# Optimization experiments

Measured on AMD Instinct MI355X. Metric: run time of the kernel, lower is better.

The kernel has to match this reference:

```python
import jax, jax.numpy as jnp
import numpy as np

N_NODES = 40000


def _sage_conv(x, edge_index, W_l, W_r, b, num_nodes):
    # PyG SAGEConv (mean aggr): out = lin_l(mean_{j in N(i)} x_j) + lin_r(x_i)
    src, dst = edge_index[0], edge_index[1]
    msgs = x[src]                                            # [E, F] gather
    sums = jax.ops.segment_sum(msgs, dst, num_segments=num_nodes)
    counts = jax.ops.segment_sum(jnp.ones((src.shape[0],), x.dtype), dst,
                                 num_segments=num_nodes)
    mean = sums / jnp.maximum(counts, 1.0)[:, None]          # [N, F]
    return mean @ W_l + b + x @ W_r


def setup_inputs() -> dict:
    key = jax.random.key(0)
    ks = jax.random.split(key, 8)
    in_c, hid_c, out_c = 128, 256, 128
    x = jax.random.normal(ks[0], (N_NODES, in_c), dtype=jnp.float32)
    edge_index = jax.random.randint(ks[1], (2, 640000), 0, N_NODES, dtype=jnp.int64)
    s1 = 1.0 / np.sqrt(in_c)
    s2 = 1.0 / np.sqrt(hid_c)
    return {
        "x": x,
        "edge_index": edge_index,
        "W1_l": jax.random.uniform(ks[2], (in_c, hid_c), jnp.float32, -s1, s1),
        "W1_r": jax.random.uniform(ks[3], (in_c, hid_c), jnp.float32, -s1, s1),
        "b1": jnp.zeros((hid_c,), jnp.float32),
        "W2_l": jax.random.uniform(ks[4], (hid_c, out_c), jnp.float32, -s2, s2),
        "W2_r": jax.random.uniform(ks[5], (hid_c, out_c), jnp.float32, -s2, s2),
        "b2": jnp.zeros((out_c,), jnp.float32),
    }


def reference(x, edge_index, W1_l, W1_r, b1, W2_l, W2_r, b2):
    h = _sage_conv(x, edge_index, W1_l, W1_r, b1, N_NODES)
    h = jax.nn.relu(h)
    out = _sage_conv(h, edge_index, W2_l, W2_r, b2, N_NODES)
    return out
```

## Files before the change

### kernel.cpp

```cpp
#include <hip/hip_runtime.h>


constexpr int F1  = 128;
constexpr int HID = 256;

typedef __attribute__((ext_vector_type(8))) short   short8;
typedef __attribute__((ext_vector_type(8))) ushort  us8;
typedef __attribute__((ext_vector_type(4))) ushort  us4;
typedef __attribute__((ext_vector_type(4))) float   f32x4;

__device__ __forceinline__ ushort f2bf(float f) {
  unsigned u = __float_as_uint(f);
  return (ushort)((u + 0x7fffu + ((u >> 16) & 1u)) >> 16);
}
__device__ __forceinline__ float bf2f_lo(unsigned v) { return __uint_as_float(v << 16); }
__device__ __forceinline__ float bf2f_hi(unsigned v) { return __uint_as_float(v & 0xffff0000u); }

__global__ void prep_kernel(const float* __restrict__ x, ushort* __restrict__ Ab,
                            int* __restrict__ deg,
                            const float* __restrict__ W1l, const float* __restrict__ W1r,
                            const float* __restrict__ W2l, const float* __restrict__ W2r,
                            ushort* __restrict__ B1t, ushort* __restrict__ B2t, int N) {
  int i = blockIdx.x * blockDim.x + threadIdx.x;
  if (i < N) deg[i] = 0;
  if (i < N * 16) {
    int row = i >> 4, c = (i & 15) * 8;
    const float* p = x + (size_t)row * F1 + c;
    us8 o;
#pragma unroll
    for (int j = 0; j < 8; ++j) o[j] = f2bf(p[j]);
    *(us8*)(Ab + (size_t)row * HID + 128 + c) = o;
    return;
  }
  int j = i - N * 16;
  if (j >= 16384) return;
  int which = j >> 13;
  int jj = j & 8191;
  int n = jj >> 5;
  int kb = (jj & 31) * 8;
  us8 o;
  if (which == 0) {
#pragma unroll
    for (int q = 0; q < 8; ++q) {
      int k = kb + q;
      float v = (k < 128) ? W1l[k * HID + n] : W1r[(k - 128) * HID + n];
      o[q] = f2bf(v);
    }
    *(us8*)(B1t + n * HID + kb) = o;
  } else {
#pragma unroll
    for (int q = 0; q < 8; ++q) {
      int k = kb + q;
      float v = (n < 128) ? W2l[k * F1 + n] : W2r[k * F1 + (n - 128)];
      o[q] = f2bf(v);
    }
    *(us8*)(B2t + n * HID + kb) = o;
  }
}

__global__ void deg_kernel(const int* __restrict__ dst, int* __restrict__ deg, int E) {
  int i = (blockIdx.x * blockDim.x + threadIdx.x) * 4;
  if (i + 3 < E) {
    int4 d = *(const int4*)(dst + i);
    atomicAdd(deg + d.x, 1);
    atomicAdd(deg + d.y, 1);
    atomicAdd(deg + d.z, 1);
    atomicAdd(deg + d.w, 1);
  } else {
    for (int q = i; q < E && q < i + 4; ++q) atomicAdd(deg + dst[q], 1);
  }
}

__global__ __launch_bounds__(256) void scan_part(const int* __restrict__ deg,
                                                 int* __restrict__ bsum, int N) {
  __shared__ int sm[256];
  int t = threadIdx.x;
  int base = blockIdx.x * 1024 + t * 4;
  int s = 0;
  if (base + 3 < N) {
    int4 v = *(const int4*)(deg + base);
    s = v.x + v.y + v.z + v.w;
  } else {
    for (int q = 0; q < 4; ++q) if (base + q < N) s += deg[base + q];
  }
  sm[t] = s;
  __syncthreads();
  for (int d = 128; d; d >>= 1) {
    if (t < d) sm[t] += sm[t + d];
    __syncthreads();
  }
  if (t == 0) bsum[blockIdx.x] = sm[0];
}

__global__ __launch_bounds__(256) void scan_emit(const int* __restrict__ deg,
                                                 const int* __restrict__ bsum,
                                                 int* __restrict__ off,
                                                 int* __restrict__ cursor, int N, int nb) {
  __shared__ int sm[256];
  __shared__ int sboff;
  int t = threadIdx.x;
  if (t < 64) {
    int v = (t < nb) ? bsum[t] : 0;
    int inc = v;
    for (int d = 1; d < 64; d <<= 1) {
      int u = __shfl_up(inc, d);
      if (t >= d) inc += u;
    }
    if (t == (int)blockIdx.x) sboff = inc - v;
    if ((int)blockIdx.x == (int)gridDim.x - 1 && t == 63) off[N] = inc;
  }
  int base = blockIdx.x * 1024 + t * 4;
  int d0 = 0, d1 = 0, d2 = 0, d3 = 0;
  if (base + 3 < N) {
    int4 v = *(const int4*)(deg + base);
    d0 = v.x; d1 = v.y; d2 = v.z; d3 = v.w;
  } else {
    if (base + 0 < N) d0 = deg[base + 0];
    if (base + 1 < N) d1 = deg[base + 1];
    if (base + 2 < N) d2 = deg[base + 2];
    if (base + 3 < N) d3 = deg[base + 3];
  }
  int s = d0 + d1 + d2 + d3;
  sm[t] = s;
  __syncthreads();
  for (int d = 1; d < 256; d <<= 1) {
    int u = (t >= d) ? sm[t - d] : 0;
    __syncthreads();
    sm[t] += u;
    __syncthreads();
  }
  int o0 = (t ? sm[t - 1] : 0) + sboff;
  int o1 = o0 + d0, o2 = o1 + d1, o3 = o2 + d2;
  if (base + 3 < N) {
    int4 o = make_int4(o0, o1, o2, o3);
    *(int4*)(off + base) = o;
    *(int4*)(cursor + base) = o;
  } else {
    if (base + 0 < N) { off[base + 0] = o0; cursor[base + 0] = o0; }
    if (base + 1 < N) { off[base + 1] = o1; cursor[base + 1] = o1; }
    if (base + 2 < N) { off[base + 2] = o2; cursor[base + 2] = o2; }
    if (base + 3 < N) { off[base + 3] = o3; cursor[base + 3] = o3; }
  }
}

__global__ void fill_kernel(const int* __restrict__ src, const int* __restrict__ dst,
                            int* __restrict__ cursor, int* __restrict__ csr, int E) {
  int i = (blockIdx.x * blockDim.x + threadIdx.x) * 2;
  if (i + 1 < E) {
    int2 d = *(const int2*)(dst + i);
    int2 s = *(const int2*)(src + i);
    int p0 = atomicAdd(cursor + d.x, 1);
    csr[p0] = s.x;
    int p1 = atomicAdd(cursor + d.y, 1);
    csr[p1] = s.y;
  } else if (i < E) {
    int p = atomicAdd(cursor + dst[i], 1);
    csr[p] = src[i];
  }
}

__device__ __forceinline__ void acc8(float* acc, const uint4 v) {
  acc[0] += bf2f_lo(v.x); acc[1] += bf2f_hi(v.x);
  acc[2] += bf2f_lo(v.y); acc[3] += bf2f_hi(v.y);
  acc[4] += bf2f_lo(v.z); acc[5] += bf2f_hi(v.z);
  acc[6] += bf2f_lo(v.w); acc[7] += bf2f_hi(v.w);
}

__global__ __launch_bounds__(256) void agg1_kernel(const int* __restrict__ off,
                                                   const int* __restrict__ csr,
                                                   ushort* __restrict__ Ab, int N) {
  const int t = threadIdx.x;
  const int w = t >> 6, l = t & 63;
  const int g = l >> 4, sub = l & 15;
  const int node = blockIdx.x * 16 + w * 4 + g;
  if (node >= N) return;
  const int s = off[node], e = off[node + 1];
  float acc[8] = {0.f, 0.f, 0.f, 0.f, 0.f, 0.f, 0.f, 0.f};
  const int cb = sub * 8;
  const int4* csr4 = (const int4*)csr;
  int k0 = s & ~7;
  int4 c0 = csr4[(k0 >> 2) + 0];
  int4 c1 = csr4[(k0 >> 2) + 1];
#define ROW1(j) (*(const uint4*)(Ab + (size_t)(j) * HID + 128 + cb))
  for (int k = k0; k < e; k += 8) {
    int4 n0 = csr4[(k >> 2) + 2];
    int4 n1 = csr4[(k >> 2) + 3];
    if (k + 0 >= s && k + 0 < e) acc8(acc, ROW1(c0.x));
    if (k + 1 >= s && k + 1 < e) acc8(acc, ROW1(c0.y));
    if (k + 2 >= s && k + 2 < e) acc8(acc, ROW1(c0.z));
    if (k + 3 >= s && k + 3 < e) acc8(acc, ROW1(c0.w));
    if (k + 4 >= s && k + 4 < e) acc8(acc, ROW1(c1.x));
    if (k + 5 >= s && k + 5 < e) acc8(acc, ROW1(c1.y));
    if (k + 6 >= s && k + 6 < e) acc8(acc, ROW1(c1.z));
    if (k + 7 < e)               acc8(acc, ROW1(c1.w));
    c0 = n0; c1 = n1;
  }
#undef ROW1
  int d = e - s; if (d < 1) d = 1;
  float inv = 1.0f / (float)d;
  us8 o;
#pragma unroll
  for (int q = 0; q < 8; ++q) o[q] = f2bf(acc[q] * inv);
  *(us8*)(Ab + (size_t)node * HID + cb) = o;
}

__global__ __launch_bounds__(256) void agg2_kernel(const ushort* __restrict__ y2,
                                                   const int* __restrict__ off,
                                                   const int* __restrict__ csr,
                                                   float* __restrict__ out, int N) {
  const int t = threadIdx.x;
  const int w = t >> 6, l = t & 63;
  const int g = l >> 4, sub = l & 15;
  const int node = blockIdx.x * 16 + w * 4 + g;
  if (node >= N) return;
  const int s = off[node], e = off[node + 1];
  float acc[8] = {0.f, 0.f, 0.f, 0.f, 0.f, 0.f, 0.f, 0.f};
  const int cb = sub * 8;
  const int4* csr4 = (const int4*)csr;
  int k0 = s & ~7;
  int4 c0 = csr4[(k0 >> 2) + 0];
  int4 c1 = csr4[(k0 >> 2) + 1];
#define ROW2(j) (*(const uint4*)(y2 + (size_t)(j) * F1 + cb))
  for (int k = k0; k < e; k += 8) {
    int4 n0 = csr4[(k >> 2) + 2];
    int4 n1 = csr4[(k >> 2) + 3];
    if (k + 0 >= s && k + 0 < e) acc8(acc, ROW2(c0.x));
    if (k + 1 >= s && k + 1 < e) acc8(acc, ROW2(c0.y));
    if (k + 2 >= s && k + 2 < e) acc8(acc, ROW2(c0.z));
    if (k + 3 >= s && k + 3 < e) acc8(acc, ROW2(c0.w));
    if (k + 4 >= s && k + 4 < e) acc8(acc, ROW2(c1.x));
    if (k + 5 >= s && k + 5 < e) acc8(acc, ROW2(c1.y));
    if (k + 6 >= s && k + 6 < e) acc8(acc, ROW2(c1.z));
    if (k + 7 < e)               acc8(acc, ROW2(c1.w));
    c0 = n0; c1 = n1;
  }
#undef ROW2
  int d = e - s; if (d < 1) d = 1;
  float inv = 1.0f / (float)d;
  float* po = out + (size_t)node * F1 + cb;
  float4 z0 = *(const float4*)(po);
  float4 z1 = *(const float4*)(po + 4);
  z0.x += acc[0] * inv; z0.y += acc[1] * inv; z0.z += acc[2] * inv; z0.w += acc[3] * inv;
  z1.x += acc[4] * inv; z1.y += acc[5] * inv; z1.z += acc[6] * inv; z1.w += acc[7] * inv;
  *(float4*)(po)     = z0;
  *(float4*)(po + 4) = z1;
}

__global__ __launch_bounds__(256) void mlp_kernel(
    const ushort* __restrict__ A, const ushort* __restrict__ B1t,
    const ushort* __restrict__ B2t, const float* __restrict__ b1,
    const float* __restrict__ b2, ushort* __restrict__ y2,
    float* __restrict__ outp, int M) {
  __shared__ __align__(16) ushort hs[64 * 256];
  const int t = threadIdx.x;
  const int l = t & 63;
  const int w = t >> 6;
  const int m0 = blockIdx.x * 64;
  const int wc = w * 64;
  const int lm = l & 15;
  const int kg = l >> 4;

  f32x4 acc[4][4];
  const f32x4 zero = {0.f, 0.f, 0.f, 0.f};
#pragma unroll
  for (int mi = 0; mi < 4; ++mi)
#pragma unroll
    for (int ni = 0; ni < 4; ++ni) acc[mi][ni] = zero;

  for (int ks = 0; ks < 8; ++ks) {
    const int kof = ks * 32 + kg * 8;
    short8 af[4], bfr[4];
#pragma unroll
    for (int i = 0; i < 4; ++i) {
      int row = m0 + i * 16 + lm; if (row >= M) row = M - 1;
      af[i]  = *(const short8*)(A + (size_t)row * HID + kof);
      bfr[i] = *(const short8*)(B1t + (size_t)(wc + i * 16 + lm) * HID + kof);
    }
#pragma unroll
    for (int mi = 0; mi < 4; ++mi)
#pragma unroll
      for (int ni = 0; ni < 4; ++ni)
        acc[mi][ni] = __builtin_amdgcn_mfma_f32_16x16x32_bf16(bfr[ni], af[mi], acc[mi][ni], 0, 0, 0);
  }

#pragma unroll
  for (int ni = 0; ni < 4; ++ni) {
    const int cn = wc + ni * 16 + (kg << 2);
    float4 bb = *(const float4*)(b1 + cn);
#pragma unroll
    for (int mi = 0; mi < 4; ++mi) {
      int row = mi * 16 + lm;
      f32x4 v = acc[mi][ni];
      unsigned p0 = (unsigned)f2bf(fmaxf(v[0] + bb.x, 0.f)) |
                    ((unsigned)f2bf(fmaxf(v[1] + bb.y, 0.f)) << 16);
      unsigned p1 = (unsigned)f2bf(fmaxf(v[2] + bb.z, 0.f)) |
                    ((unsigned)f2bf(fmaxf(v[3] + bb.w, 0.f)) << 16);
      int byte = row * 512 + ((2 * cn) ^ ((row & 7) << 4));
      uint2 pk; pk.x = p0; pk.y = p1;
      *(uint2*)((char*)hs + byte) = pk;
      acc[mi][ni] = zero;
    }
  }
  __syncthreads();

  for (int ks = 0; ks < 8; ++ks) {
    const int kof = ks * 32 + kg * 8;
    short8 af[4], bfr[4];
#pragma unroll
    for (int i = 0; i < 4; ++i) {
      int rA = i * 16 + lm;
      af[i]  = *(const short8*)((const char*)hs + rA * 512 + ((2 * kof) ^ ((rA & 7) << 4)));
      bfr[i] = *(const short8*)(B2t + (size_t)(wc + i * 16 + lm) * HID + kof);
    }
#pragma unroll
    for (int mi = 0; mi < 4; ++mi)
#pragma unroll
      for (int ni = 0; ni < 4; ++ni)
        acc[mi][ni] = __builtin_amdgcn_mfma_f32_16x16x32_bf16(bfr[ni], af[mi], acc[mi][ni], 0, 0, 0);
  }

#pragma unroll
  for (int ni = 0; ni < 4; ++ni) {
    const int cn = wc + ni * 16 + (kg << 2);
    if (wc < 128) {
#pragma unroll
      for (int mi = 0; mi < 4; ++mi) {
        int row = m0 + mi * 16 + lm;
        if (row >= M) continue;
        f32x4 v = acc[mi][ni];
        us4 o;
        o[0] = f2bf(v[0]); o[1] = f2bf(v[1]); o[2] = f2bf(v[2]); o[3] = f2bf(v[3]);
        *(us4*)(y2 + (size_t)row * F1 + cn) = o;
      }
    } else {
      float4 bb = *(const float4*)(b2 + (cn - 128));
#pragma unroll
      for (int mi = 0; mi < 4; ++mi) {
        int row = m0 + mi * 16 + lm;
        if (row >= M) continue;
        f32x4 v = acc[mi][ni];
        float4 o;
        o.x = v[0] + bb.x; o.y = v[1] + bb.y; o.z = v[2] + bb.z; o.w = v[3] + bb.w;
        *(float4*)(outp + (size_t)row * F1 + (cn - 128)) = o;
      }
    }
  }
}

extern "C" void kernel_launch(void* const* d_in, const int* in_sizes, int n_in,
                              void* d_out, int out_size, void* d_ws, size_t ws_size,
                              hipStream_t stream) {
  const float* x   = (const float*)d_in[0];
  const int* edge  = (const int*)d_in[1];
  const float* W1l = (const float*)d_in[2];
  const float* W1r = (const float*)d_in[3];
  const float* b1  = (const float*)d_in[4];
  const float* W2l = (const float*)d_in[5];
  const float* W2r = (const float*)d_in[6];
  const float* b2  = (const float*)d_in[7];
  float* out = (float*)d_out;

  const int N = in_sizes[0] / F1;
  const int E = in_sizes[1] / 2;
  const int* src = edge;
  const int* dst = edge + E;

  uintptr_t p = (uintptr_t)d_ws;
  auto alloc = [&](size_t bytes) -> void* {
    void* r = (void*)p;
    p += (bytes + 255) & ~(size_t)255;
    return r;
  };
  int* deg      = (int*)alloc((size_t)N * 4);
  int* off      = (int*)alloc((size_t)(N + 1) * 4);
  int* cursor   = (int*)alloc((size_t)N * 4);
  int* csr      = (int*)alloc((size_t)(E + 16) * 4);
  int* bsum     = (int*)alloc(64 * 4);
  ushort* Abf   = (ushort*)alloc((size_t)N * HID * 2);
  ushort* y2    = (ushort*)alloc((size_t)N * F1 * 2);
  ushort* B1t   = (ushort*)alloc((size_t)HID * HID * 2);
  ushort* B2t   = (ushort*)alloc((size_t)HID * HID * 2);
  (void)ws_size; (void)n_in; (void)out_size;

  prep_kernel<<<(N * 16 + 16384 + 255) / 256, 256, 0, stream>>>(
      x, Abf, deg, W1l, W1r, W2l, W2r, B1t, B2t, N);
  deg_kernel<<<(E / 4 + 255) / 256, 256, 0, stream>>>(dst, deg, E);

  const int nb = (N + 1023) / 1024;
  scan_part<<<nb, 256, 0, stream>>>(deg, bsum, N);
  scan_emit<<<nb, 256, 0, stream>>>(deg, bsum, off, cursor, N, nb);

  fill_kernel<<<(E / 2 + 255) / 256, 256, 0, stream>>>(src, dst, cursor, csr, E);
  agg1_kernel<<<(N + 15) / 16, 256, 0, stream>>>(off, csr, Abf, N);

  mlp_kernel<<<(N + 63) / 64, 256, 0, stream>>>(Abf, B1t, B2t, b1, b2, y2, out, N);

  agg2_kernel<<<(N + 15) / 16, 256, 0, stream>>>(y2, off, csr, out, N);
}
```

Measured before the change: 251.6 us.

## Halve MLP row tile and double-buffer fragment loads across K steps

The fused two-layer MLP kernel now processes 32 rows per block instead of 64, doubling the grid (about 1250 blocks) and halving accumulator registers and shared memory. It also software-pipelines the K loop, prefetching the next step's A/B fragments into alternate register buffers while MFMAs run on the current ones. The aim is more occupancy and latency hiding for global loads. In exchange, each B weight fragment is reused across fewer rows, so weight traffic per output doubles.

```diff
diff --git a/kernel.cpp b/kernel.cpp
--- a/kernel.cpp
+++ b/kernel.cpp
@@ -251,36 +251,58 @@
     const ushort* __restrict__ B2t, const float* __restrict__ b1,
     const float* __restrict__ b2, ushort* __restrict__ y2,
     float* __restrict__ outp, int M) {
-  __shared__ __align__(16) ushort hs[64 * 256];
+  __shared__ __align__(16) ushort hs[32 * 256];
   const int t = threadIdx.x;
   const int l = t & 63;
   const int w = t >> 6;
-  const int m0 = blockIdx.x * 64;
+  const int m0 = blockIdx.x * 32;
   const int wc = w * 64;
   const int lm = l & 15;
   const int kg = l >> 4;
 
-  f32x4 acc[4][4];
+  f32x4 acc[2][4];
   const f32x4 zero = {0.f, 0.f, 0.f, 0.f};
 #pragma unroll
-  for (int mi = 0; mi < 4; ++mi)
+  for (int mi = 0; mi < 2; ++mi)
 #pragma unroll
     for (int ni = 0; ni < 4; ++ni) acc[mi][ni] = zero;
 
-  for (int ks = 0; ks < 8; ++ks) {
-    const int kof = ks * 32 + kg * 8;
-    short8 af[4], bfr[4];
-#pragma unroll
-    for (int i = 0; i < 4; ++i) {
-      int row = m0 + i * 16 + lm; if (row >= M) row = M - 1;
-      af[i]  = *(const short8*)(A + (size_t)row * HID + kof);
-      bfr[i] = *(const short8*)(B1t + (size_t)(wc + i * 16 + lm) * HID + kof);
-    }
-#pragma unroll
-    for (int mi = 0; mi < 4; ++mi)
-#pragma unroll
-      for (int ni = 0; ni < 4; ++ni)
-        acc[mi][ni] = __builtin_amdgcn_mfma_f32_16x16x32_bf16(bfr[ni], af[mi], acc[mi][ni], 0, 0, 0);
+#define LOAD_P1(AF, BF, KOF)                                                       \
+  {                                                                                \
+    const int kof_ = (KOF);                                                        \
+    _Pragma("unroll")                                                              \
+    for (int i_ = 0; i_ < 2; ++i_) {                                               \
+      int row_ = m0 + i_ * 16 + lm; if (row_ >= M) row_ = M - 1;                   \
+      AF[i_] = *(const short8*)(A + (size_t)row_ * HID + kof_);                    \
+    }                                                                              \
+    _Pragma("unroll")                                                              \
+    for (int n_ = 0; n_ < 4; ++n_)                                                 \
+      BF[n_] = *(const short8*)(B1t + (size_t)(wc + n_ * 16 + lm) * HID + kof_);   \
+  }
+
+#define FMA_2x4(AF, BF)                                                            \
+  {                                                                                \
+    _Pragma("unroll")                                                              \
+    for (int mi_ = 0; mi_ < 2; ++mi_)                                              \
+      _Pragma("unroll")                                                            \
+      for (int ni_ = 0; ni_ < 4; ++ni_)                                            \
+        acc[mi_][ni_] = __builtin_amdgcn_mfma_f32_16x16x32_bf16(                   \
+            BF[ni_], AF[mi_], acc[mi_][ni_], 0, 0, 0);                             \
+  }
+
+  {
+    short8 afA[2], bfA[4], afB[2], bfB[4];
+    LOAD_P1(afA, bfA, kg * 8);
+#pragma unroll
+    for (int ks = 0; ks < 8; ++ks) {
+      if ((ks & 1) == 0) {
+        if (ks < 7) LOAD_P1(afB, bfB, (ks + 1) * 32 + kg * 8);
+        FMA_2x4(afA, bfA);
+      } else {
+        if (ks < 7) LOAD_P1(afA, bfA, (ks + 1) * 32 + kg * 8);
+        FMA_2x4(afB, bfB);
+      }
+    }
   }
 
 #pragma unroll
@@ -288,7 +310,7 @@
     const int cn = wc + ni * 16 + (kg << 2);
     float4 bb = *(const float4*)(b1 + cn);
 #pragma unroll
-    for (int mi = 0; mi < 4; ++mi) {
+    for (int mi = 0; mi < 2; ++mi) {
       int row = mi * 16 + lm;
       f32x4 v = acc[mi][ni];
       unsigned p0 = (unsigned)f2bf(fmaxf(v[0] + bb.x, 0.f)) |
@@ -303,20 +325,34 @@
   }
   __syncthreads();
 
-  for (int ks = 0; ks < 8; ++ks) {
-    const int kof = ks * 32 + kg * 8;
-    short8 af[4], bfr[4];
-#pragma unroll
-    for (int i = 0; i < 4; ++i) {
-      int rA = i * 16 + lm;
-      af[i]  = *(const short8*)((const char*)hs + rA * 512 + ((2 * kof) ^ ((rA & 7) << 4)));
-      bfr[i] = *(const short8*)(B2t + (size_t)(wc + i * 16 + lm) * HID + kof);
-    }
-#pragma unroll
-    for (int mi = 0; mi < 4; ++mi)
-#pragma unroll
-      for (int ni = 0; ni < 4; ++ni)
-        acc[mi][ni] = __builtin_amdgcn_mfma_f32_16x16x32_bf16(bfr[ni], af[mi], acc[mi][ni], 0, 0, 0);
+#define LOAD_B2(BF, KOF)                                                           \
+  {                                                                                \
+    const int kof_ = (KOF);                                                        \
+    _Pragma("unroll")                                                              \
+    for (int n_ = 0; n_ < 4; ++n_)                                                 \
+      BF[n_] = *(const short8*)(B2t + (size_t)(wc + n_ * 16 + lm) * HID + kof_);   \
+  }
+
+  {
+    short8 bfA[4], bfB[4];
+    LOAD_B2(bfA, kg * 8);
+#pragma unroll
+    for (int ks = 0; ks < 8; ++ks) {
+      const int kof = ks * 32 + kg * 8;
+      short8 afL[2];
+#pragma unroll
+      for (int i = 0; i < 2; ++i) {
+        int rA = i * 16 + lm;
+        afL[i] = *(const short8*)((const char*)hs + rA * 512 + ((2 * kof) ^ ((rA & 7) << 4)));
+      }
+      if ((ks & 1) == 0) {
+        if (ks < 7) LOAD_B2(bfB, (ks + 1) * 32 + kg * 8);
+        FMA_2x4(afL, bfA);
+      } else {
+        if (ks < 7) LOAD_B2(bfA, (ks + 1) * 32 + kg * 8);
+        FMA_2x4(afL, bfB);
+      }
+    }
   }
 
 #pragma unroll
@@ -324,7 +360,7 @@
     const int cn = wc + ni * 16 + (kg << 2);
     if (wc < 128) {
 #pragma unroll
-      for (int mi = 0; mi < 4; ++mi) {
+      for (int mi = 0; mi < 2; ++mi) {
         int row = m0 + mi * 16 + lm;
         if (row >= M) continue;
         f32x4 v = acc[mi][ni];
@@ -335,7 +371,7 @@
     } else {
       float4 bb = *(const float4*)(b2 + (cn - 128));
 #pragma unroll
-      for (int mi = 0; mi < 4; ++mi) {
+      for (int mi = 0; mi < 2; ++mi) {
         int row = m0 + mi * 16 + lm;
         if (row >= M) continue;
         f32x4 v = acc[mi][ni];
@@ -345,6 +381,9 @@
       }
     }
   }
+#undef LOAD_P1
+#undef LOAD_B2
+#undef FMA_2x4
 }
 
 extern "C" void kernel_launch(void* const* d_in, const int* in_sizes, int n_in,
@@ -393,7 +432,7 @@
   fill_kernel<<<(E / 2 + 255) / 256, 256, 0, stream>>>(src, dst, cursor, csr, E);
   agg1_kernel<<<(N + 15) / 16, 256, 0, stream>>>(off, csr, Abf, N);
 
-  mlp_kernel<<<(N + 63) / 64, 256, 0, stream>>>(Abf, B1t, B2t, b1, b2, y2, out, N);
+  mlp_kernel<<<(N + 31) / 32, 256, 0, stream>>>(Abf, B1t, B2t, b1, b2, y2, out, N);
 
   agg2_kernel<<<(N + 15) / 16, 256, 0, stream>>>(y2, off, csr, out, N);
 }
```

After: 258.0 us. 1.03x slower.
